# Kernel optimization log

Measured on AMD Instinct MI355X. Metric: run time of the kernel, lower is better.

Reference implementation:

```python
import jax, jax.numpy as jnp
import numpy as np

N, K, CIN, COUT = 150000, 27, 128, 128


def setup_inputs() -> dict:
    key = jax.random.key(0)
    k1, k2, k3 = jax.random.split(key, 3)
    data = jax.random.normal(k1, (N, CIN), dtype=jnp.float32)
    weights = jax.random.normal(k2, (COUT, K, CIN), dtype=jnp.float32) * 0.05
    # neighbour indices in [-1, N): -1 marks empty octree neighbours (~1/151 here)
    neighbour = jax.random.randint(k3, (N, K), 0, N + 1, dtype=jnp.int64) - 1
    return {"data": data, "weights": weights, "neighbour": neighbour}


def reference(data, weights, neighbour):
    """Octree sparse conv: out[m] = sum_k W[:,k,:] @ data[neigh[m,k]] (0 if -1).

    Scans over the 27 kernel offsets so the [N,K,Cin] gather is never
    materialized; each step is a masked row-gather + dense GEMM.
    """
    w_k = jnp.transpose(weights, (1, 2, 0))   # [K, Cin, Cout]
    n_k = neighbour.T                          # [K, N]

    def body(acc, xs):
        w, idx = xs                            # [Cin, Cout], [N]
        valid = (idx >= 0)[:, None]            # [N, 1]
        g = jnp.where(valid, data[jnp.clip(idx, 0, None)], 0.0)  # [N, Cin]
        return acc + g @ w, None

    out0 = jnp.zeros((data.shape[0], w_k.shape[-1]), dtype=data.dtype)
    out, _ = jax.lax.scan(body, out0, (w_k, n_k))
    return out
```

## Files before the change

### kernel.cpp

```cpp
#include <hip/hip_runtime.h>

#define N_PTS 150000
#define NK 27
#define CIN 128
#define COUT 128
#define BM 128
#define NBLK ((N_PTS + BM - 1) / BM)

typedef __attribute__((ext_vector_type(8))) short bfrag8;
typedef __attribute__((ext_vector_type(4))) float facc4;

__device__ inline unsigned short f2bf(float f) {
    unsigned u = __builtin_bit_cast(unsigned, f);
    u += 0x7FFFu + ((u >> 16) & 1u);
    return (unsigned short)(u >> 16);
}
__device__ inline unsigned pack2(float a, float b) {
    return (unsigned)f2bf(a) | ((unsigned)f2bf(b) << 16);
}
__device__ inline void glds16(const void* g, void* l) {
    __builtin_amdgcn_global_load_lds(
        (const __attribute__((address_space(1))) void*)g,
        (__attribute__((address_space(3))) void*)l, 16, 0, 0);
}

__global__ void cast_data_kernel(const float* __restrict__ in,
                                 unsigned short* __restrict__ out) {
    const int n8_data = N_PTS * (CIN / 8);
    const int n8_all  = (N_PTS + 1) * (CIN / 8);
    int i = blockIdx.x * blockDim.x + threadIdx.x;
    int stride = gridDim.x * blockDim.x;
    for (; i < n8_all; i += stride) {
        uint4 v;
        if (i < n8_data) {
            const float4* p = (const float4*)(in + (size_t)i * 8);
            float4 x = p[0], y = p[1];
            v.x = pack2(x.x, x.y); v.y = pack2(x.z, x.w);
            v.z = pack2(y.x, y.y); v.w = pack2(y.z, y.w);
        } else {
            v.x = v.y = v.z = v.w = 0u;
        }
        *(uint4*)(out + (size_t)i * 8) = v;
    }
}

__global__ void prep_weights_h(const float* __restrict__ w,
                               unsigned short* __restrict__ wkh) {
    int i = blockIdx.x * blockDim.x + threadIdx.x;
    if (i >= NK * 2 * 128 * 8) return;
    int bu = i & 7, co = (i >> 3) & 127, h = (i >> 10) & 1, k = i >> 11;
    int ci = h * 64 + (bu ^ (co & 7)) * 8;
    const float4* src = (const float4*)(w + ((size_t)co * NK + k) * CIN + ci);
    float4 x = src[0], y = src[1];
    uint4 v;
    v.x = pack2(x.x, x.y); v.y = pack2(x.z, x.w);
    v.z = pack2(y.x, y.y); v.w = pack2(y.z, y.w);
    ((uint4*)wkh)[i] = v;
}


#define STAGE_A(Q, ADST)                                                     \
  {                                                                          \
    const int k_  = (Q) >> 1;                                                \
    const int hb_ = ((Q) & 1) << 7;                                          \
    int iv0 = *(const int*)(ldsI + s0 * 108 + k_ * 4);                       \
    int iv1 = *(const int*)(ldsI + s1 * 108 + k_ * 4);                       \
    size_t e0 = (s0ok && iv0 >= 0) ? (size_t)iv0 : (size_t)N_PTS;            \
    size_t e1 = (s1ok && iv1 >= 0) ? (size_t)iv1 : (size_t)N_PTS;            \
    glds16(dbfB + e0 * 256 + hb_ + aswz, (ADST) + s0 * 128 + lu16);          \
    glds16(dbfB + e1 * 256 + hb_ + aswz, (ADST) + s1 * 128 + lu16);          \
  }

#define STAGE_B(Q, BDST)                                                     \
  {                                                                          \
    const char* bs_ = wkhB + (size_t)(Q) * 16384 + t * 16;                   \
    glds16(bs_,        (BDST) + t * 16);                                     \
    glds16(bs_ + 8192, (BDST) + t * 16 + 8192);                              \
  }

#define MFMA_PHASE(ABUF, BBUF)                                                      \
  {                                                                                 \
    __builtin_amdgcn_s_setprio(1);                                                  \
    _Pragma("unroll")                                                               \
    for (int kk = 0; kk < 2; ++kk) {                                                \
      const int sw_ = (((kk * 4 + lk) ^ (lr & 7)) << 4);                            \
      bfrag8 a0 = *(const bfrag8*)((ABUF) + (wrow * 32 + lr) * 128 + sw_);          \
      bfrag8 a1 = *(const bfrag8*)((ABUF) + (wrow * 32 + 16 + lr) * 128 + sw_);     \
      _Pragma("unroll")                                                             \
      for (int ct = 0; ct < 4; ++ct) {                                              \
        bfrag8 b = *(const bfrag8*)((BBUF) + (h * 64 + ct * 16 + lr) * 128 + sw_);  \
        acc[0][ct] = __builtin_amdgcn_mfma_f32_16x16x32_bf16(a0, b, acc[0][ct],     \
                                                             0, 0, 0);              \
        acc[1][ct] = __builtin_amdgcn_mfma_f32_16x16x32_bf16(a1, b, acc[1][ct],     \
                                                             0, 0, 0);              \
      }                                                                             \
    }                                                                               \
    __builtin_amdgcn_s_setprio(0);                                                  \
  }

#define WAIT_BAR(N)                                                          \
    __builtin_amdgcn_sched_barrier(0);                                       \
    asm volatile("s_waitcnt vmcnt(" #N ")" ::: "memory");                    \
    __builtin_amdgcn_s_barrier();                                            \
    __builtin_amdgcn_sched_barrier(0);

__global__ __launch_bounds__(512, 4)
void octconv_v10(const unsigned short* __restrict__ dbf,
                 const unsigned short* __restrict__ wkh,
                 const int* __restrict__ nbr,
                 float* __restrict__ out) {
    __shared__ __align__(1024) unsigned char lds[2 * 16384 + 2 * 16384 + 13824];

    const int t = threadIdx.x;
    const int w = t >> 6, l = t & 63;
    const int lr = l & 15, lk = l >> 4;
    const int h = w & 1, wrow = w >> 1;
    const int m0 = blockIdx.x * BM;

    const int lu   = l & 7;
    const int lu16 = lu * 16;
    const int s0 = t >> 3;
    const int s1 = s0 + 64;
    const bool s0ok = (m0 + s0) < N_PTS;
    const bool s1ok = (m0 + s1) < N_PTS;
    const int aswz = (lu ^ (s0 & 7)) << 4;

    const char* dbfB = (const char*)dbf;
    const char* wkhB = (const char*)wkh;
    char* a0p = (char*)lds;
    char* a1p = (char*)lds + 16384;
    char* b0p = (char*)lds + 32768;
    char* b1p = (char*)lds + 49152;
    char* ldsI = (char*)lds + 65536;

    facc4 acc[2][4];
    const facc4 fz = {0.f, 0.f, 0.f, 0.f};
#pragma unroll
    for (int a = 0; a < 2; ++a)
#pragma unroll
        for (int b = 0; b < 4; ++b) acc[a][b] = fz;

    {
        const char* nsrc = (const char*)nbr + (size_t)m0 * 108;
        const int rows_valid = (N_PTS - m0) < BM ? (N_PTS - m0) : BM;
        const int nlimit = rows_valid * 108;
        int o;
        o = t * 16;        if (o < nlimit) glds16(nsrc + o, ldsI + o);
        o = 8192 + t * 16; if (t < 352 && o < nlimit) glds16(nsrc + o, ldsI + o);
    }
    WAIT_BAR(0)

    STAGE_A(0, a0p)
    STAGE_B(0, b0p)
    WAIT_BAR(0)

#pragma unroll 1
    for (int p = 0; p <= 52; ++p) {
        STAGE_B(p + 1, b1p)
        STAGE_A(p + 1, a1p)
        MFMA_PHASE(a0p, b0p)
        WAIT_BAR(0)
        { char* tp = a0p; a0p = a1p; a1p = tp; }
        { char* tp = b0p; b0p = b1p; b1p = tp; }
    }

    MFMA_PHASE(a0p, b0p)

#pragma unroll
    for (int rt = 0; rt < 2; ++rt) {
        const int r0 = m0 + wrow * 32 + rt * 16 + lk * 4;
#pragma unroll
        for (int ct = 0; ct < 4; ++ct) {
#pragma unroll
            for (int r = 0; r < 4; ++r) {
                int row = r0 + r;
                if (row < N_PTS)
                    out[(size_t)row * COUT + h * 64 + ct * 16 + lr] = acc[rt][ct][r];
            }
        }
    }
}

__global__ void naive_kernel(const float* __restrict__ data, const float* __restrict__ wgt,
                             const int* __restrict__ nbr, float* __restrict__ out) {
    int mm = blockIdx.x;
    int co = threadIdx.x;
    if (mm >= N_PTS) return;
    float acc = 0.f;
    for (int k = 0; k < NK; ++k) {
        int idx = nbr[mm * NK + k];
        if (idx < 0) continue;
        const float* d  = data + (size_t)idx * CIN;
        const float* wp = wgt + ((size_t)co * NK + k) * CIN;
        for (int ci = 0; ci < CIN; ++ci) acc += d[ci] * wp[ci];
    }
    out[(size_t)mm * COUT + co] = acc;
}

extern "C" void kernel_launch(void* const* d_in, const int* in_sizes, int n_in,
                              void* d_out, int out_size, void* d_ws, size_t ws_size,
                              hipStream_t stream) {
    const float* data = (const float*)d_in[0];
    const float* wgt  = (const float*)d_in[1];
    const int*   nbr  = (const int*)d_in[2];
    float*       out  = (float*)d_out;

    const size_t wk_bytes  = (size_t)NK * 2 * 128 * 8 * 16;
    const size_t dbf_bytes = (size_t)(N_PTS + 1) * CIN * 2;

    if (ws_size < wk_bytes + dbf_bytes) {
        naive_kernel<<<N_PTS, COUT, 0, stream>>>(data, wgt, nbr, out);
        return;
    }
    unsigned short* wkh = (unsigned short*)d_ws;
    unsigned short* dbf = (unsigned short*)((char*)d_ws + wk_bytes);

    prep_weights_h<<<(NK * 2 * 128 * 8 + 255) / 256, 256, 0, stream>>>(wgt, wkh);
    cast_data_kernel<<<2048, 256, 0, stream>>>(data, dbf);

    octconv_v10<<<NBLK, 512, 0, stream>>>(dbf, wkh, nbr, out);
}
```

Before: 189.0 us.

## Triple-buffer A gather with register-prefetched neighbour indices and transposed index table

Replaces the LDS-staged neighbour index tile with per-thread index loads from global memory, prefetched into registers several stages ahead. An extra transpose kernel lays the index table out k-major so these loads coalesce. The A-tile gather moves from double to triple buffering, keeping two gathers in flight (waitcnt 4 instead of 0) so gather latency overlaps the MFMA phase. The cost is a separate transpose launch, extra workspace, and more LDS per block (80KB vs ~78KB), which may lower occupancy.

After: 209.7 us. +11.0%, slower.

```diff
diff --git a/kernel.cpp b/kernel.cpp
--- a/kernel.cpp
+++ b/kernel.cpp
@@ -58,15 +58,36 @@
     ((uint4*)wkh)[i] = v;
 }
 
-
-#define STAGE_A(Q, ADST)                                                     \
+__global__ void transpose_nbr(const int* __restrict__ nbr, int* __restrict__ nbrT) {
+    __shared__ int tile[256 * NK];
+    const int t  = threadIdx.x;
+    const int m0 = blockIdx.x * 256;
+    const int base = m0 * NK;
+    for (int i = t; i < 256 * NK; i += 256) {
+        int g = base + i;
+        tile[i] = (g < N_PTS * NK) ? nbr[g] : -1;
+    }
+    __syncthreads();
+    const int row = m0 + t;
+    if (row < N_PTS) {
+#pragma unroll
+        for (int k = 0; k < NK; ++k) nbrT[k * N_PTS + row] = tile[t * NK + k];
+    }
+}
+
+
+#define LOAD_IV(G, IV0, IV1)                                                 \
   {                                                                          \
-    const int k_  = (Q) >> 1;                                                \
+    const int kq_ = (G) >> 1;                                                \
+    IV0 = nbrS[(size_t)kq_ * kStr + (size_t)r0c * rStr];                     \
+    IV1 = nbrS[(size_t)kq_ * kStr + (size_t)r1c * rStr];                     \
+  }
+
+#define STAGE_A(Q, ADST, IV0, IV1)                                           \
+  {                                                                          \
     const int hb_ = ((Q) & 1) << 7;                                          \
-    int iv0 = *(const int*)(ldsI + s0 * 108 + k_ * 4);                       \
-    int iv1 = *(const int*)(ldsI + s1 * 108 + k_ * 4);                       \
-    size_t e0 = (s0ok && iv0 >= 0) ? (size_t)iv0 : (size_t)N_PTS;            \
-    size_t e1 = (s1ok && iv1 >= 0) ? (size_t)iv1 : (size_t)N_PTS;            \
+    size_t e0 = (s0ok && (IV0) >= 0) ? (size_t)(IV0) : (size_t)N_PTS;        \
+    size_t e1 = (s1ok && (IV1) >= 0) ? (size_t)(IV1) : (size_t)N_PTS;        \
     glds16(dbfB + e0 * 256 + hb_ + aswz, (ADST) + s0 * 128 + lu16);          \
     glds16(dbfB + e1 * 256 + hb_ + aswz, (ADST) + s1 * 128 + lu16);          \
   }
@@ -104,12 +125,17 @@
     __builtin_amdgcn_s_barrier();                                            \
     __builtin_amdgcn_sched_barrier(0);
 
+#define ROTATE_BUFS                                                          \
+    { char* tp = pAr; pAr = pAm; pAm = pAw; pAw = tp; }                      \
+    { char* tp = pBr; pBr = pBw; pBw = tp; }
+
 __global__ __launch_bounds__(512, 4)
-void octconv_v10(const unsigned short* __restrict__ dbf,
+void octconv_v11(const unsigned short* __restrict__ dbf,
                  const unsigned short* __restrict__ wkh,
-                 const int* __restrict__ nbr,
+                 const int* __restrict__ nbrS,
+                 const int kStr, const int rStr,
                  float* __restrict__ out) {
-    __shared__ __align__(1024) unsigned char lds[2 * 16384 + 2 * 16384 + 13824];
+    __shared__ __align__(1024) unsigned char lds[3 * 16384 + 2 * 16384];
 
     const int t = threadIdx.x;
     const int w = t >> 6, l = t & 63;
@@ -123,15 +149,17 @@
     const int s1 = s0 + 64;
     const bool s0ok = (m0 + s0) < N_PTS;
     const bool s1ok = (m0 + s1) < N_PTS;
+    const int r0c = (m0 + s0) < N_PTS ? (m0 + s0) : (N_PTS - 1);
+    const int r1c = (m0 + s1) < N_PTS ? (m0 + s1) : (N_PTS - 1);
     const int aswz = (lu ^ (s0 & 7)) << 4;
 
     const char* dbfB = (const char*)dbf;
     const char* wkhB = (const char*)wkh;
-    char* a0p = (char*)lds;
-    char* a1p = (char*)lds + 16384;
-    char* b0p = (char*)lds + 32768;
-    char* b1p = (char*)lds + 49152;
-    char* ldsI = (char*)lds + 65536;
+    char* pAr = (char*)lds;
+    char* pAm = (char*)lds + 16384;
+    char* pAw = (char*)lds + 32768;
+    char* pBr = (char*)lds + 49152;
+    char* pBw = (char*)lds + 65536;
 
     facc4 acc[2][4];
     const facc4 fz = {0.f, 0.f, 0.f, 0.f};
@@ -140,31 +168,35 @@
 #pragma unroll
         for (int b = 0; b < 4; ++b) acc[a][b] = fz;
 
-    {
-        const char* nsrc = (const char*)nbr + (size_t)m0 * 108;
-        const int rows_valid = (N_PTS - m0) < BM ? (N_PTS - m0) : BM;
-        const int nlimit = rows_valid * 108;
-        int o;
-        o = t * 16;        if (o < nlimit) glds16(nsrc + o, ldsI + o);
-        o = 8192 + t * 16; if (t < 352 && o < nlimit) glds16(nsrc + o, ldsI + o);
-    }
+    int ivA0, ivA1, ivB0, ivB1, ivc0, ivc1, ivn0, ivn1;
+    LOAD_IV(0, ivA0, ivA1)
+    LOAD_IV(1, ivB0, ivB1)
+    LOAD_IV(2, ivc0, ivc1)
+    STAGE_A(0, pAr, ivA0, ivA1)
+    STAGE_B(0, pBr)
+    STAGE_A(1, pAm, ivB0, ivB1)
+    WAIT_BAR(2)
+
+#pragma unroll 1
+    for (int p = 0; p <= 50; ++p) {
+        STAGE_B(p + 1, pBw)
+        STAGE_A(p + 2, pAw, ivc0, ivc1)
+        MFMA_PHASE(pAr, pBr)
+        LOAD_IV(p + 3, ivn0, ivn1)
+        WAIT_BAR(4)
+        ROTATE_BUFS
+        ivc0 = ivn0; ivc1 = ivn1;
+    }
+    STAGE_B(52, pBw)
+    STAGE_A(53, pAw, ivc0, ivc1)
+    MFMA_PHASE(pAr, pBr)
+    WAIT_BAR(2)
+    ROTATE_BUFS
+    STAGE_B(53, pBw)
+    MFMA_PHASE(pAr, pBr)
     WAIT_BAR(0)
-
-    STAGE_A(0, a0p)
-    STAGE_B(0, b0p)
-    WAIT_BAR(0)
-
-#pragma unroll 1
-    for (int p = 0; p <= 52; ++p) {
-        STAGE_B(p + 1, b1p)
-        STAGE_A(p + 1, a1p)
-        MFMA_PHASE(a0p, b0p)
-        WAIT_BAR(0)
-        { char* tp = a0p; a0p = a1p; a1p = tp; }
-        { char* tp = b0p; b0p = b1p; b1p = tp; }
-    }
-
-    MFMA_PHASE(a0p, b0p)
+    ROTATE_BUFS
+    MFMA_PHASE(pAr, pBr)
 
 #pragma unroll
     for (int rt = 0; rt < 2; ++rt) {
@@ -205,8 +237,9 @@
     const int*   nbr  = (const int*)d_in[2];
     float*       out  = (float*)d_out;
 
-    const size_t wk_bytes  = (size_t)NK * 2 * 128 * 8 * 16;
-    const size_t dbf_bytes = (size_t)(N_PTS + 1) * CIN * 2;
+    const size_t wk_bytes   = (size_t)NK * 2 * 128 * 8 * 16;
+    const size_t dbf_bytes  = (size_t)(N_PTS + 1) * CIN * 2;
+    const size_t nbrT_bytes = (size_t)NK * N_PTS * 4;
 
     if (ws_size < wk_bytes + dbf_bytes) {
         naive_kernel<<<N_PTS, COUT, 0, stream>>>(data, wgt, nbr, out);
@@ -218,5 +251,11 @@
     prep_weights_h<<<(NK * 2 * 128 * 8 + 255) / 256, 256, 0, stream>>>(wgt, wkh);
     cast_data_kernel<<<2048, 256, 0, stream>>>(data, dbf);
 
-    octconv_v10<<<NBLK, 512, 0, stream>>>(dbf, wkh, nbr, out);
-}
+    if (ws_size >= wk_bytes + dbf_bytes + nbrT_bytes) {
+        int* nbrT = (int*)((char*)d_ws + wk_bytes + dbf_bytes);
+        transpose_nbr<<<(N_PTS + 255) / 256, 256, 0, stream>>>(nbr, nbrT);
+        octconv_v11<<<NBLK, 512, 0, stream>>>(dbf, wkh, nbrT, N_PTS, 1, out);
+    } else {
+        octconv_v11<<<NBLK, 512, 0, stream>>>(dbf, wkh, nbr, 1, NK, out);
+    }
+}
```

## Load weight fragments directly into registers and triple-buffer gathered rows in LDS

Applied to the files above, without the earlier changes.

Weights are pre-packed into per-lane MFMA fragment order, so each wave loads its B fragments straight from global memory into registers (double-buffered bx/by) instead of staging them through LDS. The freed LDS is used to triple-buffer the gathered A rows, and partial vmcnt waits let loads for two stages ahead stay in flight across the barrier. This removes LDS traffic and bank pressure for the B operand and gives the gather more time to land. In exchange it uses more VGPRs (16 uint4 of B data per thread), which may hurt occupancy at 512 threads per block, and the waitcnt counts must exactly match the number of outstanding loads.

Result: slower. 239.2 us (+26.5%).

```diff
diff --git a/kernel.cpp b/kernel.cpp
--- a/kernel.cpp
+++ b/kernel.cpp
@@ -44,18 +44,24 @@
     }
 }
 
-__global__ void prep_weights_h(const float* __restrict__ w,
-                               unsigned short* __restrict__ wkh) {
+__global__ void prep_weights_frag2(const float* __restrict__ w,
+                                   unsigned short* __restrict__ wkf) {
     int i = blockIdx.x * blockDim.x + threadIdx.x;
-    if (i >= NK * 2 * 128 * 8) return;
-    int bu = i & 7, co = (i >> 3) & 127, h = (i >> 10) & 1, k = i >> 11;
-    int ci = h * 64 + (bu ^ (co & 7)) * 8;
+    if (i >= 54 * 2 * 4 * 2 * 64) return;
+    int l  = i & 63;
+    int kk = (i >> 6) & 1;
+    int ct = (i >> 7) & 3;
+    int h  = (i >> 9) & 1;
+    int q  = i >> 10;
+    int k  = q >> 1, h2 = q & 1;
+    int co = h * 64 + ct * 16 + (l & 15);
+    int ci = h2 * 64 + kk * 32 + (l >> 4) * 8;
     const float4* src = (const float4*)(w + ((size_t)co * NK + k) * CIN + ci);
     float4 x = src[0], y = src[1];
     uint4 v;
     v.x = pack2(x.x, x.y); v.y = pack2(x.z, x.w);
     v.z = pack2(y.x, y.y); v.w = pack2(y.z, y.w);
-    ((uint4*)wkh)[i] = v;
+    ((uint4*)wkf)[i] = v;
 }
 
 
@@ -71,14 +77,15 @@
     glds16(dbfB + e1 * 256 + hb_ + aswz, (ADST) + s1 * 128 + lu16);          \
   }
 
-#define STAGE_B(Q, BDST)                                                     \
+#define ISSUE_B(Q, BSET)                                                     \
   {                                                                          \
-    const char* bs_ = wkhB + (size_t)(Q) * 16384 + t * 16;                   \
-    glds16(bs_,        (BDST) + t * 16);                                     \
-    glds16(bs_ + 8192, (BDST) + t * 16 + 8192);                              \
+    const char* bs_ = wkfB + (size_t)(Q) * 16384 + h * 8192 + l * 16;        \
+    _Pragma("unroll")                                                        \
+    for (int j_ = 0; j_ < 8; ++j_)                                           \
+      BSET[j_] = *(const uint4*)(bs_ + j_ * 1024);                           \
   }
 
-#define MFMA_PHASE(ABUF, BBUF)                                                      \
+#define MFMA_PHASE_R(ABUF, BSET)                                                    \
   {                                                                                 \
     __builtin_amdgcn_s_setprio(1);                                                  \
     _Pragma("unroll")                                                               \
@@ -88,7 +95,7 @@
       bfrag8 a1 = *(const bfrag8*)((ABUF) + (wrow * 32 + 16 + lr) * 128 + sw_);     \
       _Pragma("unroll")                                                             \
       for (int ct = 0; ct < 4; ++ct) {                                              \
-        bfrag8 b = *(const bfrag8*)((BBUF) + (h * 64 + ct * 16 + lr) * 128 + sw_);  \
+        bfrag8 b = __builtin_bit_cast(bfrag8, BSET[ct * 2 + kk]);                   \
         acc[0][ct] = __builtin_amdgcn_mfma_f32_16x16x32_bf16(a0, b, acc[0][ct],     \
                                                              0, 0, 0);              \
         acc[1][ct] = __builtin_amdgcn_mfma_f32_16x16x32_bf16(a1, b, acc[1][ct],     \
@@ -104,12 +111,15 @@
     __builtin_amdgcn_s_barrier();                                            \
     __builtin_amdgcn_sched_barrier(0);
 
+#define ROTATE_A                                                             \
+    { char* tp = pA0; pA0 = pA1; pA1 = pA2; pA2 = tp; }
+
 __global__ __launch_bounds__(512, 4)
-void octconv_v10(const unsigned short* __restrict__ dbf,
-                 const unsigned short* __restrict__ wkh,
+void octconv_v12(const unsigned short* __restrict__ dbf,
+                 const unsigned short* __restrict__ wkf,
                  const int* __restrict__ nbr,
                  float* __restrict__ out) {
-    __shared__ __align__(1024) unsigned char lds[2 * 16384 + 2 * 16384 + 13824];
+    __shared__ __align__(1024) unsigned char lds[3 * 16384 + 13824];
 
     const int t = threadIdx.x;
     const int w = t >> 6, l = t & 63;
@@ -126,12 +136,11 @@
     const int aswz = (lu ^ (s0 & 7)) << 4;
 
     const char* dbfB = (const char*)dbf;
-    const char* wkhB = (const char*)wkh;
-    char* a0p = (char*)lds;
-    char* a1p = (char*)lds + 16384;
-    char* b0p = (char*)lds + 32768;
-    char* b1p = (char*)lds + 49152;
-    char* ldsI = (char*)lds + 65536;
+    const char* wkfB = (const char*)wkf;
+    char* pA0 = (char*)lds;
+    char* pA1 = (char*)lds + 16384;
+    char* pA2 = (char*)lds + 32768;
+    char* ldsI = (char*)lds + 49152;
 
     facc4 acc[2][4];
     const facc4 fz = {0.f, 0.f, 0.f, 0.f};
@@ -139,6 +148,8 @@
     for (int a = 0; a < 2; ++a)
 #pragma unroll
         for (int b = 0; b < 4; ++b) acc[a][b] = fz;
+
+    uint4 bx[8], by[8];
 
     {
         const char* nsrc = (const char*)nbr + (size_t)m0 * 108;
@@ -150,21 +161,31 @@
     }
     WAIT_BAR(0)
 
-    STAGE_A(0, a0p)
-    STAGE_B(0, b0p)
-    WAIT_BAR(0)
+    ISSUE_B(0, bx)
+    STAGE_A(0, pA0)
+    STAGE_A(1, pA1)
+    WAIT_BAR(2)
 
 #pragma unroll 1
-    for (int p = 0; p <= 52; ++p) {
-        STAGE_B(p + 1, b1p)
-        STAGE_A(p + 1, a1p)
-        MFMA_PHASE(a0p, b0p)
-        WAIT_BAR(0)
-        { char* tp = a0p; a0p = a1p; a1p = tp; }
-        { char* tp = b0p; b0p = b1p; b1p = tp; }
-    }
-
-    MFMA_PHASE(a0p, b0p)
+    for (int kp = 0; kp <= 25; ++kp) {
+        const int p = 2 * kp;
+        STAGE_A(p + 2, pA2)
+        ISSUE_B(p + 1, by)
+        MFMA_PHASE_R(pA0, bx)
+        WAIT_BAR(10)
+        ROTATE_A
+        STAGE_A(p + 3, pA2)
+        ISSUE_B(p + 2, bx)
+        MFMA_PHASE_R(pA0, by)
+        WAIT_BAR(10)
+        ROTATE_A
+    }
+
+    ISSUE_B(53, by)
+    MFMA_PHASE_R(pA0, bx)
+    WAIT_BAR(8)
+    ROTATE_A
+    MFMA_PHASE_R(pA0, by)
 
 #pragma unroll
     for (int rt = 0; rt < 2; ++rt) {
@@ -205,18 +226,18 @@
     const int*   nbr  = (const int*)d_in[2];
     float*       out  = (float*)d_out;
 
-    const size_t wk_bytes  = (size_t)NK * 2 * 128 * 8 * 16;
+    const size_t wk_bytes  = (size_t)54 * 2 * 4 * 2 * 64 * 16;
     const size_t dbf_bytes = (size_t)(N_PTS + 1) * CIN * 2;
 
     if (ws_size < wk_bytes + dbf_bytes) {
         naive_kernel<<<N_PTS, COUT, 0, stream>>>(data, wgt, nbr, out);
         return;
     }
-    unsigned short* wkh = (unsigned short*)d_ws;
+    unsigned short* wkf = (unsigned short*)d_ws;
     unsigned short* dbf = (unsigned short*)((char*)d_ws + wk_bytes);
 
-    prep_weights_h<<<(NK * 2 * 128 * 8 + 255) / 256, 256, 0, stream>>>(wgt, wkh);
+    prep_weights_frag2<<<(54 * 2 * 4 * 2 * 64 + 255) / 256, 256, 0, stream>>>(wgt, wkf);
     cast_data_kernel<<<2048, 256, 0, stream>>>(data, dbf);
 
-    octconv_v10<<<NBLK, 512, 0, stream>>>(dbf, wkh, nbr, out);
-}
+    octconv_v12<<<NBLK, 512, 0, stream>>>(dbf, wkf, nbr, out);
+}
```

## Triple-buffer gathered A tiles with prefetch distance two and register-held indices

Applied to the files above, without the earlier changes.

The gathered activation tiles move from double to triple buffering, so each A stage is issued two phases ahead. The barrier waits only until all but the newest two loads have landed instead of draining every load. The neighbour indices for each thread's two rows are loaded once into registers, replacing the per-stage LDS reads, and the main loop is fully unrolled with a fixed buffer rotation. The goal is to hide gather latency behind the MFMA work. The cost is 54 extra live index registers under a 512x4 launch bound, which could cause spills, plus a larger code footprint.

After: 182.7 us, median of 2. 3.3% less time.

```diff
diff --git a/kernel.cpp b/kernel.cpp
--- a/kernel.cpp
+++ b/kernel.cpp
@@ -61,10 +61,9 @@
 
 #define STAGE_A(Q, ADST)                                                     \
   {                                                                          \
-    const int k_  = (Q) >> 1;                                                \
     const int hb_ = ((Q) & 1) << 7;                                          \
-    int iv0 = *(const int*)(ldsI + s0 * 108 + k_ * 4);                       \
-    int iv1 = *(const int*)(ldsI + s1 * 108 + k_ * 4);                       \
+    int iv0 = iA[(Q) >> 1];                                                  \
+    int iv1 = iB[(Q) >> 1];                                                  \
     size_t e0 = (s0ok && iv0 >= 0) ? (size_t)iv0 : (size_t)N_PTS;            \
     size_t e1 = (s1ok && iv1 >= 0) ? (size_t)iv1 : (size_t)N_PTS;            \
     glds16(dbfB + e0 * 256 + hb_ + aswz, (ADST) + s0 * 128 + lu16);          \
@@ -104,12 +103,26 @@
     __builtin_amdgcn_s_barrier();                                            \
     __builtin_amdgcn_sched_barrier(0);
 
+#define PH_STD(Q, AR, AW, BR, BW)                                            \
+    STAGE_B((Q) + 1, BW)                                                     \
+    STAGE_A((Q) + 2, AW)                                                     \
+    MFMA_PHASE(AR, BR)                                                       \
+    WAIT_BAR(2)
+
+#define GROUP6(P)                                                            \
+    PH_STD((P) + 0, pA0, pA2, pB0, pB1)                                      \
+    PH_STD((P) + 1, pA1, pA0, pB1, pB0)                                      \
+    PH_STD((P) + 2, pA2, pA1, pB0, pB1)                                      \
+    PH_STD((P) + 3, pA0, pA2, pB1, pB0)                                      \
+    PH_STD((P) + 4, pA1, pA0, pB0, pB1)                                      \
+    PH_STD((P) + 5, pA2, pA1, pB1, pB0)
+
 __global__ __launch_bounds__(512, 4)
-void octconv_v10(const unsigned short* __restrict__ dbf,
+void octconv_v13(const unsigned short* __restrict__ dbf,
                  const unsigned short* __restrict__ wkh,
                  const int* __restrict__ nbr,
                  float* __restrict__ out) {
-    __shared__ __align__(1024) unsigned char lds[2 * 16384 + 2 * 16384 + 13824];
+    __shared__ __align__(1024) unsigned char lds[3 * 16384 + 2 * 16384];
 
     const int t = threadIdx.x;
     const int w = t >> 6, l = t & 63;
@@ -127,11 +140,11 @@
 
     const char* dbfB = (const char*)dbf;
     const char* wkhB = (const char*)wkh;
-    char* a0p = (char*)lds;
-    char* a1p = (char*)lds + 16384;
-    char* b0p = (char*)lds + 32768;
-    char* b1p = (char*)lds + 49152;
-    char* ldsI = (char*)lds + 65536;
+    char* pA0 = (char*)lds;
+    char* pA1 = (char*)lds + 16384;
+    char* pA2 = (char*)lds + 32768;
+    char* pB0 = (char*)lds + 49152;
+    char* pB1 = (char*)lds + 65536;
 
     facc4 acc[2][4];
     const facc4 fz = {0.f, 0.f, 0.f, 0.f};
@@ -140,31 +153,36 @@
 #pragma unroll
         for (int b = 0; b < 4; ++b) acc[a][b] = fz;
 
+    int iA[27], iB[27];
     {
-        const char* nsrc = (const char*)nbr + (size_t)m0 * 108;
-        const int rows_valid = (N_PTS - m0) < BM ? (N_PTS - m0) : BM;
-        const int nlimit = rows_valid * 108;
-        int o;
-        o = t * 16;        if (o < nlimit) glds16(nsrc + o, ldsI + o);
-        o = 8192 + t * 16; if (t < 352 && o < nlimit) glds16(nsrc + o, ldsI + o);
-    }
+        const int r0 = (m0 + s0) < N_PTS ? (m0 + s0) : (N_PTS - 1);
+        const int r1 = (m0 + s1) < N_PTS ? (m0 + s1) : (N_PTS - 1);
+        const int* p0 = nbr + (size_t)r0 * NK;
+        const int* p1 = nbr + (size_t)r1 * NK;
+#pragma unroll
+        for (int j = 0; j < 27; ++j) iA[j] = p0[j];
+#pragma unroll
+        for (int j = 0; j < 27; ++j) iB[j] = p1[j];
+    }
+
+    STAGE_A(0, pA0)
+    STAGE_B(0, pB0)
+    STAGE_A(1, pA1)
+    WAIT_BAR(2)
+
+    GROUP6(0)  GROUP6(6)  GROUP6(12) GROUP6(18)
+    GROUP6(24) GROUP6(30) GROUP6(36) GROUP6(42)
+
+    PH_STD(48, pA0, pA2, pB0, pB1)
+    PH_STD(49, pA1, pA0, pB1, pB0)
+    PH_STD(50, pA2, pA1, pB0, pB1)
+    PH_STD(51, pA0, pA2, pB1, pB0)
+
+    STAGE_B(53, pB1)
+    MFMA_PHASE(pA1, pB0)
     WAIT_BAR(0)
 
-    STAGE_A(0, a0p)
-    STAGE_B(0, b0p)
-    WAIT_BAR(0)
-
-#pragma unroll 1
-    for (int p = 0; p <= 52; ++p) {
-        STAGE_B(p + 1, b1p)
-        STAGE_A(p + 1, a1p)
-        MFMA_PHASE(a0p, b0p)
-        WAIT_BAR(0)
-        { char* tp = a0p; a0p = a1p; a1p = tp; }
-        { char* tp = b0p; b0p = b1p; b1p = tp; }
-    }
-
-    MFMA_PHASE(a0p, b0p)
+    MFMA_PHASE(pA2, pB1)
 
 #pragma unroll
     for (int rt = 0; rt < 2; ++rt) {
@@ -218,5 +236,5 @@
     prep_weights_h<<<(NK * 2 * 128 * 8 + 255) / 256, 256, 0, stream>>>(wgt, wkh);
     cast_data_kernel<<<2048, 256, 0, stream>>>(data, dbf);
 
-    octconv_v10<<<NBLK, 512, 0, stream>>>(dbf, wkh, nbr, out);
-}
+    octconv_v13<<<NBLK, 512, 0, stream>>>(dbf, wkh, nbr, out);
+}
```
